# Performance work log

Hardware: AMD Instinct MI355X
Metric: run time of the kernel (lower is better)

## Reference

```python
import jax, jax.numpy as jnp
import numpy as np

B, L, D, S = 64, 512, 768, 8
HOP, LAMB = 3, 0.5


def _layernorm(x, g, b, eps=1e-5):
    m = x.mean(-1, keepdims=True)
    v = x.var(-1, keepdims=True)
    return (x - m) / jnp.sqrt(v + eps) * g + b


def _hop_refine(cur, sentence, ln_g, ln_b):
    # cur, sentence: [B,S,D]. HOP-1 refinement steps, then return last row.
    for _ in range(HOP - 1):
        coef = jnp.einsum('bd,bsd->bs', cur[:, -1, :], sentence)  # [B,S]
        a = coef[..., None] * sentence                             # [B,S,D]
        cur = LAMB * _layernorm(jax.nn.sigmoid(a), ln_g, ln_b) + sentence
    return cur[:, -1, :]  # [B,D]


def _conv1d(x, w, b):
    # x: [B,D,S], w: [Dout,Din,3], padding=1 (same)
    y = jax.lax.conv_general_dilated(
        x, w, window_strides=(1,), padding=((1, 1),),
        dimension_numbers=('NCH', 'OIH', 'NCH'))
    return y + b[None, :, None]


def setup_inputs() -> dict:
    key = jax.random.key(0)
    ks = jax.random.split(key, 16)
    p = lambda k, shp: (jax.random.normal(k, shp, dtype=jnp.float32) * 0.02)
    # segment boundaries: strictly increasing, start at 1, <= L, gaps ~63 with jitter < 32
    base = 1 + np.arange(S + 1) * ((L - 1) // S)          # [9]
    jitter = np.array(jax.random.randint(ks[15], (B, S + 1), 0, 32))
    jitter[:, 0] = 0
    jitter[:, -1] = 0
    seg_bounds = jnp.asarray(base[None, :] + jitter, dtype=jnp.int64 if jax.config.jax_enable_x64 else jnp.int32)
    return {
        'bert_output': jax.random.normal(ks[0], (B, L, D), dtype=jnp.float32),
        'target': jax.random.normal(ks[1], (B, D), dtype=jnp.float32),
        'gc1_w': p(ks[2], (D, D)), 'gc1_b': p(ks[3], (D,)),
        'gc2_w': p(ks[4], (D, D)), 'gc2_b': p(ks[5], (D,)),
        'conv1_w': p(ks[6], (D, D, 3)), 'conv1_b': p(ks[7], (D,)),
        'conv2_w': p(ks[8], (D, D, 3)), 'conv2_b': p(ks[9], (D,)),
        'ln_g': jnp.ones((D,), jnp.float32), 'ln_b': jnp.zeros((D,), jnp.float32),
        'fc2_w': p(ks[10], (3 * D, 3)), 'fc2_b': p(ks[11], (3,)),
        'seg_bounds': seg_bounds,
    }


def reference(bert_output, target, gc1_w, gc1_b, gc2_w, gc2_b,
              conv1_w, conv1_b, conv2_w, conv2_b, ln_g, ln_b,
              fc2_w, fc2_b, seg_bounds):
    dt = bert_output.dtype
    start = seg_bounds[:, :-1]   # [B,S]
    end = seg_bounds[:, 1:]      # [B,S]
    pos = jnp.arange(L)
    seg_mask = ((pos[None, None, :] >= start[:, :, None]) &
                (pos[None, None, :] < end[:, :, None])).astype(dt)  # [B,S,L]
    cnt = (end - start).astype(dt)                                   # [B,S]
    # batched segment-mean pooling
    sentence = jnp.einsum('bsl,bld->bsd', seg_mask, bert_output) / cnt[..., None]

    # GCN branch: adj = I + superdiagonal, row-degree normalization
    adj = jnp.eye(S, dtype=dt) + jnp.eye(S, k=1, dtype=dt)
    denom = adj.sum(axis=1)  # [S]

    def gcn(x, w, b):
        h = jnp.einsum('bsd,de->bse', x, w)
        return jnp.einsum('st,btd->bsd', adj, h) / denom[None, :, None] + b

    g1 = jnp.tanh(gcn(sentence, gc1_w, gc1_b))
    g2 = jnp.tanh(gcn(g1, gc2_w, gc2_b))
    a3 = _hop_refine(g2, sentence, ln_g, ln_b)

    # Conv branch: two conv1d (k=3, pad=1) over the segment axis
    x = jnp.swapaxes(sentence, 1, 2)  # [B,D,S]
    c = jnp.tanh(_conv1d(x, conv1_w, conv1_b))
    c = jnp.tanh(_conv1d(c, conv2_w, conv2_b))
    conv_out = jnp.swapaxes(c, 1, 2)  # [B,S,D]
    a4 = _hop_refine(conv_out, sentence, ln_g, ln_b)

    # Self-mask branch
    coef0 = jnp.einsum('bd,bsd->bs', sentence[:, -1, :], sentence)
    tmask = jax.nn.sigmoid(coef0[..., None] * sentence)
    a5 = _hop_refine(tmask, sentence, ln_g, ln_b)

    fnout = jnp.stack([a3, a4, a5], axis=1)                 # [B,3,D]
    # NOTE: original uses target[0] (first sample's pooler output) for all samples
    w = jax.nn.softmax(jnp.einsum('bkd,d->bk', fnout, target[0]), axis=1)
    fn = (fnout * w[..., None]).reshape(fnout.shape[0], 3 * D)
    return fn @ fc2_w + fc2_b  # [B,3]
```

## Files before the change

kernel.cpp:

```cpp
#include <hip/hip_runtime.h>


typedef unsigned short u16;
typedef short short8 __attribute__((ext_vector_type(8)));
typedef float f32x4 __attribute__((ext_vector_type(4)));

#define PART 147456

__device__ __forceinline__ float bf2f(u16 h) {
    unsigned int u = ((unsigned int)h) << 16;
    float f;
    __builtin_memcpy(&f, &u, 4);
    return f;
}
__device__ __forceinline__ u16 f2bf(float f) {
    unsigned int u;
    __builtin_memcpy(&u, &f, 4);
    u = (u + 0x7fffu + ((u >> 16) & 1u)) >> 16;
    return (u16)u;
}
__device__ __forceinline__ float sigm(float x) { return 1.0f / (1.0f + __expf(-x)); }
__device__ __forceinline__ float ftanh(float x) {
    const float xc = fminf(fmaxf(x, -15.0f), 15.0f);
    const float e = __expf(2.0f * xc);
    return __fdividef(e - 1.0f, e + 1.0f);
}
__device__ __forceinline__ float ldv(const void* p, long i, bool bf) {
    return bf ? bf2f(((const u16*)p)[i]) : ((const float*)p)[i];
}

__device__ __forceinline__ bool detect_bf16(const u16* bert) {
    int hits = 0;
#pragma unroll
    for (int i = 0; i < 256; i += 2) {
        const int e = (bert[i] >> 7) & 0xFF;
        hits += (e >= 115 && e <= 130) ? 1 : 0;
    }
    return hits > 64;
}

__global__ __launch_bounds__(256) void k1_pool_pack(
    const void* __restrict__ bertv, const int* __restrict__ sb,
    const void* __restrict__ c1w, const void* __restrict__ c2w,
    float* __restrict__ sentP, float* __restrict__ accs,
    u16* __restrict__ W1pack, u16* __restrict__ W2pack)
{
    const int u = blockIdx.x, t = threadIdx.x;
    if (u >= 768) {
        const int o = u - 768;
        const bool bf = detect_bf16((const u16*)bertv);
#pragma unroll
        for (int j = 0; j < 3; ++j) {
            const int i = t + 256 * j;
            const long base = (long)(o * 768 + i) * 3;
            u16 w1[3], w2[3];
            if (bf) {
                const u16* p1 = (const u16*)c1w + base;
                const u16* p2 = (const u16*)c2w + base;
                w1[0] = p1[0]; w1[1] = p1[1]; w1[2] = p1[2];
                w2[0] = p2[0]; w2[1] = p2[1]; w2[2] = p2[2];
            } else {
                const float* p1 = (const float*)c1w + base;
                const float* p2 = (const float*)c2w + base;
                w1[0] = f2bf(p1[0]); w1[1] = f2bf(p1[1]); w1[2] = f2bf(p1[2]);
                w2[0] = f2bf(p2[0]); w2[1] = f2bf(p2[1]); w2[2] = f2bf(p2[2]);
            }
            u16* d1 = W1pack + (size_t)o * 2304 + i;
            d1[0] = w1[0]; d1[768] = w1[1]; d1[1536] = w1[2];
            u16* d2 = W2pack + (size_t)o * 1536 + i;
            d2[0] = w2[0]; d2[768] = w2[1];
        }
        return;
    }
    if (u < 256 && t < 240)
        ((float4*)accs)[u * 240 + t] = make_float4(0.f, 0.f, 0.f, 0.f);
    const bool bf = detect_bf16((const u16*)bertv);
    const bool is64 = (sb[1] == 0);
    const int q = u & 3, w = u >> 2;
    const int b = w / 3, si = w - 3 * (w / 3), s = 5 + si;
    const int i0 = b * 9 + s, i1 = i0 + 1;
    int st = is64 ? sb[2 * i0] : sb[i0];
    int en = is64 ? sb[2 * i1] : sb[i1];
    st = st < 0 ? 0 : (st > 511 ? 511 : st);
    en = en <= st ? st + 1 : (en > 512 ? 512 : en);
    const int n = en - st;
    const int r0 = st + (n * q) / 4;
    const int r1 = st + (n * (q + 1)) / 4;
    float a0 = 0.f, a1 = 0.f, a2 = 0.f;
    if (bf) {
        const u16* base = (const u16*)bertv + (size_t)b * 512 * 768;
        int l = r0;
        for (; l + 3 < r1; l += 4) {
            const u16* p0 = base + (size_t)l * 768;
#pragma unroll
            for (int rr = 0; rr < 4; ++rr) {
                const u16* p = p0 + rr * 768;
                a0 += bf2f(p[t]);
                a1 += bf2f(p[t + 256]);
                a2 += bf2f(p[t + 512]);
            }
        }
        for (; l < r1; ++l) {
            const u16* p = base + (size_t)l * 768;
            a0 += bf2f(p[t]);
            a1 += bf2f(p[t + 256]);
            a2 += bf2f(p[t + 512]);
        }
    } else {
        const float* base = (const float*)bertv + (size_t)b * 512 * 768;
        int l = r0;
        for (; l + 3 < r1; l += 4) {
            const float* p0 = base + (size_t)l * 768;
#pragma unroll
            for (int rr = 0; rr < 4; ++rr) {
                const float* p = p0 + rr * 768;
                a0 += p[t];
                a1 += p[t + 256];
                a2 += p[t + 512];
            }
        }
        for (; l < r1; ++l) {
            const float* p = base + (size_t)l * 768;
            a0 += p[t];
            a1 += p[t + 256];
            a2 += p[t + 512];
        }
    }
    const float inv = 1.0f / (float)n;
    float* o = sentP + (size_t)q * PART + b * 2304 + si * 768;
    o[t] = a0 * inv;
    o[t + 256] = a1 * inv;
    o[t + 512] = a2 * inv;
}

template <int XMODE, int WMODE, int NPART>
__device__ __forceinline__ void gemm_core(
    const float* __restrict__ x, int xstride, const void* __restrict__ bias,
    const void* __restrict__ W, int wstride, bool bf,
    float* __restrict__ out, int ostride,
    int n0, int k0, u16* As, u16* Bs)
{
    const int t = threadIdx.x;
    const int r = t >> 2;
    const int cseg = (t & 3) * 32;
    const int wave = t >> 6, lane = t & 63;
    const int lm = lane & 15, lq = lane >> 4;
    f32x4 acc[4] = {};

    for (int kk = 0; kk < 256; kk += 128) {
        const int kg = k0 + kk;
        {
            const float* xp = x + (size_t)r * xstride + (kg + cseg);
            u16* dst = As + r * 136 + cseg;
#pragma unroll
            for (int i = 0; i < 8; ++i) {
                float4 v = ((const float4*)xp)[i];
                if (NPART == 4) {
                    const float4 v1 = ((const float4*)(xp + PART))[i];
                    const float4 v2 = ((const float4*)(xp + 2 * PART))[i];
                    const float4 v3 = ((const float4*)(xp + 3 * PART))[i];
                    v.x += v1.x + v2.x + v3.x;
                    v.y += v1.y + v2.y + v3.y;
                    v.z += v1.z + v2.z + v3.z;
                    v.w += v1.w + v2.w + v3.w;
                }
                if (XMODE == 1) {
                    int kb = kg + cseg + i * 4;
                    if (kb >= 768) kb -= 768;
                    v.x = ftanh(v.x + ldv(bias, kb, bf));
                    v.y = ftanh(v.y + ldv(bias, kb + 1, bf));
                    v.z = ftanh(v.z + ldv(bias, kb + 2, bf));
                    v.w = ftanh(v.w + ldv(bias, kb + 3, bf));
                }
                ((ushort4*)dst)[i] = make_ushort4(f2bf(v.x), f2bf(v.y), f2bf(v.z), f2bf(v.w));
            }
        }
        if (WMODE == 0) {
            const int p = t >> 2;
            const int nseg = (t & 3) * 16;
            u16 q0[16], q1[16];
            if (bf) {
                const u16* w0 = (const u16*)W + (size_t)(kg + 2 * p) * 768 + n0 + nseg;
                ((uint4*)q0)[0] = ((const uint4*)w0)[0];
                ((uint4*)q0)[1] = ((const uint4*)w0)[1];
                ((uint4*)q1)[0] = ((const uint4*)(w0 + 768))[0];
                ((uint4*)q1)[1] = ((const uint4*)(w0 + 768))[1];
            } else {
                const float* w0 = (const float*)W + (size_t)(kg + 2 * p) * 768 + n0 + nseg;
#pragma unroll
                for (int e = 0; e < 4; ++e) {
                    float4 v0 = ((const float4*)w0)[e];
                    float4 v1 = ((const float4*)(w0 + 768))[e];
                    q0[4 * e] = f2bf(v0.x); q0[4 * e + 1] = f2bf(v0.y);
                    q0[4 * e + 2] = f2bf(v0.z); q0[4 * e + 3] = f2bf(v0.w);
                    q1[4 * e] = f2bf(v1.x); q1[4 * e + 1] = f2bf(v1.y);
                    q1[4 * e + 2] = f2bf(v1.z); q1[4 * e + 3] = f2bf(v1.w);
                }
            }
#pragma unroll
            for (int e = 0; e < 16; ++e)
                *(ushort2*)(Bs + (nseg + e) * 136 + 2 * p) = make_ushort2(q0[e], q1[e]);
        } else {
            const u16* wp = (const u16*)W + (size_t)(n0 + r) * wstride + kg + cseg;
            u16* dst = Bs + r * 136 + cseg;
#pragma unroll
            for (int i = 0; i < 4; ++i)
                ((uint4*)dst)[i] = ((const uint4*)wp)[i];
        }
        __syncthreads();
        const u16* ap = As + (wave * 16 + lm) * 136 + lq * 8;
        const u16* bp = Bs + lm * 136 + lq * 8;
#pragma unroll
        for (int ks = 0; ks < 4; ++ks) {
            short8 af = *(const short8*)(ap + ks * 32);
#pragma unroll
            for (int nf = 0; nf < 4; ++nf) {
                short8 bfr = *(const short8*)(bp + nf * 16 * 136 + ks * 32);
                acc[nf] = __builtin_amdgcn_mfma_f32_16x16x32_bf16(af, bfr, acc[nf], 0, 0, 0);
            }
        }
        __syncthreads();
    }
#pragma unroll
    for (int nf = 0; nf < 4; ++nf) {
#pragma unroll
        for (int rg = 0; rg < 4; ++rg) {
            const int row = wave * 16 + lq * 4 + rg;
            const int col = n0 + nf * 16 + lm;
            atomicAdd(out + (size_t)row * ostride + col, acc[nf][rg]);
        }
    }
}

__global__ __launch_bounds__(256) void k2_gemm_a(
    const void* __restrict__ bertv,
    const float* __restrict__ sentP, const void* __restrict__ gc1w,
    const u16* __restrict__ W1pack, float* __restrict__ g1acc, float* __restrict__ c1acc)
{
    __shared__ u16 As[64 * 136];
    __shared__ u16 Bs[64 * 136];
    const bool bf = detect_bf16((const u16*)bertv);
    const int u = blockIdx.x;
    if (u < 36) {
        gemm_core<0, 0, 4>(sentP + 1536, 2304, nullptr, gc1w, 768, bf, g1acc, 768,
                           (u / 3) * 64, (u % 3) * 256, As, Bs);
    } else if (u < 144) {
        const int v = u - 36;
        gemm_core<0, 2, 4>(sentP, 2304, nullptr, W1pack, 2304, bf, c1acc, 1536,
                           (v / 9) * 64, (v % 9) * 256, As, Bs);
    } else {
        const int v = u - 144;
        gemm_core<0, 2, 4>(sentP + 768, 2304, nullptr, W1pack, 2304, bf, c1acc + 768, 1536,
                           (v / 6) * 64, (v % 6) * 256, As, Bs);
    }
}

__global__ __launch_bounds__(256) void k3_gemm_b(
    const void* __restrict__ bertv,
    const float* __restrict__ g1acc, const float* __restrict__ c1acc,
    const void* __restrict__ gc2w, const u16* __restrict__ W2pack,
    const void* __restrict__ gc1b, const void* __restrict__ c1b,
    float* __restrict__ g2acc, float* __restrict__ c2acc)
{
    __shared__ u16 As[64 * 136];
    __shared__ u16 Bs[64 * 136];
    const bool bf = detect_bf16((const u16*)bertv);
    const int u = blockIdx.x;
    if (u < 36) {
        gemm_core<1, 0, 1>(g1acc, 768, gc1b, gc2w, 768, bf, g2acc, 768,
                           (u / 3) * 64, (u % 3) * 256, As, Bs);
    } else {
        const int v = u - 36;
        gemm_core<1, 2, 1>(c1acc, 1536, c1b, W2pack, 1536, bf, c2acc, 768,
                           (v / 6) * 64, (v % 6) * 256, As, Bs);
    }
}

__device__ __forceinline__ float block_sum(float v, float* red) {
#pragma unroll
    for (int m = 1; m < 64; m <<= 1) v += __shfl_xor(v, m, 64);
    const int wave = threadIdx.x >> 6, lane = threadIdx.x & 63;
    if (lane == 0) red[wave] = v;
    __syncthreads();
    const float r = red[0] + red[1] + red[2] + red[3];
    __syncthreads();
    return r;
}

__global__ __launch_bounds__(256) void k4_final(
    const void* __restrict__ bertv,
    const float* __restrict__ sentP, const float* __restrict__ g2acc,
    const float* __restrict__ c2acc,
    const void* __restrict__ gc2b, const void* __restrict__ c2b,
    const void* __restrict__ lng, const void* __restrict__ lnb,
    const void* __restrict__ target, const void* __restrict__ fc2w,
    const void* __restrict__ fc2b, void* __restrict__ outp)
{
    __shared__ float red[4];
    const bool bf = detect_bf16((const u16*)bertv);
    const int t = threadIdx.x, b = blockIdx.x;
    float s_[3], g_[3], bb_[3];
    const float* sp = sentP + b * 2304 + 1536;
#pragma unroll
    for (int i = 0; i < 3; ++i) {
        const int d = t + 256 * i;
        s_[i] = sp[d] + sp[PART + d] + sp[2 * PART + d] + sp[3 * PART + d];
        g_[i] = ldv(lng, d, bf);
        bb_[i] = ldv(lnb, d, bf);
    }

    auto refine2 = [&](float* yv) {
#pragma unroll
        for (int it = 0; it < 2; ++it) {
            const float c = block_sum(yv[0] * s_[0] + yv[1] * s_[1] + yv[2] * s_[2], red);
            float tt[3], sm = 0.0f, sq = 0.0f;
#pragma unroll
            for (int i = 0; i < 3; ++i) {
                tt[i] = sigm(c * s_[i]);
                sm += tt[i];
                sq += tt[i] * tt[i];
            }
            const float m = block_sum(sm, red) * (1.0f / 768.0f);
            const float q = block_sum(sq, red) * (1.0f / 768.0f);
            const float inv = rsqrtf(fmaxf(q - m * m, 0.0f) + 1e-5f);
#pragma unroll
            for (int i = 0; i < 3; ++i)
                yv[i] = 0.5f * ((tt[i] - m) * inv * g_[i] + bb_[i]) + s_[i];
        }
    };

    float a3[3], a4[3], a5[3], y[3];
#pragma unroll
    for (int i = 0; i < 3; ++i) {
        const int d = t + 256 * i;
        y[i] = ftanh(g2acc[b * 768 + d] + ldv(gc2b, d, bf));
    }
    refine2(y);
    a3[0] = y[0]; a3[1] = y[1]; a3[2] = y[2];
#pragma unroll
    for (int i = 0; i < 3; ++i) {
        const int d = t + 256 * i;
        y[i] = ftanh(c2acc[b * 768 + d] + ldv(c2b, d, bf));
    }
    refine2(y);
    a4[0] = y[0]; a4[1] = y[1]; a4[2] = y[2];
    const float ss = block_sum(s_[0] * s_[0] + s_[1] * s_[1] + s_[2] * s_[2], red);
#pragma unroll
    for (int i = 0; i < 3; ++i) y[i] = sigm(ss * s_[i]);
    refine2(y);
    a5[0] = y[0]; a5[1] = y[1]; a5[2] = y[2];

    float tg[3];
#pragma unroll
    for (int i = 0; i < 3; ++i) tg[i] = ldv(target, t + 256 * i, bf);
    const float u0 = block_sum(a3[0] * tg[0] + a3[1] * tg[1] + a3[2] * tg[2], red);
    const float u1 = block_sum(a4[0] * tg[0] + a4[1] * tg[1] + a4[2] * tg[2], red);
    const float u2 = block_sum(a5[0] * tg[0] + a5[1] * tg[1] + a5[2] * tg[2], red);
    const float mx = fmaxf(u0, fmaxf(u1, u2));
    const float e0 = __expf(u0 - mx), e1 = __expf(u1 - mx), e2 = __expf(u2 - mx);
    const float es = e0 + e1 + e2;
    const float w0 = e0 / es, w1 = e1 / es, w2 = e2 / es;

    float p0 = 0.0f, p1 = 0.0f, p2 = 0.0f;
#pragma unroll
    for (int i = 0; i < 3; ++i) {
        const int d = t + 256 * i;
        const float va = w0 * a3[i], vb = w1 * a4[i], vc = w2 * a5[i];
        p0 += va * ldv(fc2w, d * 3 + 0, bf) + vb * ldv(fc2w, (768 + d) * 3 + 0, bf) + vc * ldv(fc2w, (1536 + d) * 3 + 0, bf);
        p1 += va * ldv(fc2w, d * 3 + 1, bf) + vb * ldv(fc2w, (768 + d) * 3 + 1, bf) + vc * ldv(fc2w, (1536 + d) * 3 + 1, bf);
        p2 += va * ldv(fc2w, d * 3 + 2, bf) + vb * ldv(fc2w, (768 + d) * 3 + 2, bf) + vc * ldv(fc2w, (1536 + d) * 3 + 2, bf);
    }
    p0 = block_sum(p0, red);
    p1 = block_sum(p1, red);
    p2 = block_sum(p2, red);
    if (t == 0) {
        const float o0 = p0 + ldv(fc2b, 0, bf);
        const float o1 = p1 + ldv(fc2b, 1, bf);
        const float o2 = p2 + ldv(fc2b, 2, bf);
        if (bf) {
            ((u16*)outp)[b * 3 + 0] = f2bf(o0);
            ((u16*)outp)[b * 3 + 1] = f2bf(o1);
            ((u16*)outp)[b * 3 + 2] = f2bf(o2);
        } else {
            ((float*)outp)[b * 3 + 0] = o0;
            ((float*)outp)[b * 3 + 1] = o1;
            ((float*)outp)[b * 3 + 2] = o2;
        }
    }
}

extern "C" void kernel_launch(void* const* d_in, const int* in_sizes, int n_in,
                              void* d_out, int out_size, void* d_ws, size_t ws_size,
                              hipStream_t stream) {
    const void* bert   = d_in[0];
    const void* target = d_in[1];
    const void* gc1w   = d_in[2];
    const void* gc1b   = d_in[3];
    const void* gc2w   = d_in[4];
    const void* gc2b   = d_in[5];
    const void* c1w    = d_in[6];
    const void* c1b    = d_in[7];
    const void* c2w    = d_in[8];
    const void* c2b    = d_in[9];
    const void* lng    = d_in[10];
    const void* lnb    = d_in[11];
    const void* fc2w   = d_in[12];
    const void* fc2b   = d_in[13];
    const int*  sb     = (const int*)d_in[14];

    float* sentP  = (float*)d_ws;
    float* accs   = sentP + 4 * PART;
    float* g1acc  = accs;
    float* c1acc  = accs + 49152;
    float* g2acc  = c1acc + 98304;
    float* c2acc  = g2acc + 49152;
    u16*   W1pack = (u16*)(accs + 245760);
    u16*   W2pack = W1pack + 768 * 2304;

    k1_pool_pack<<<1536, 256, 0, stream>>>(bert, sb, c1w, c2w, sentP, accs, W1pack, W2pack);
    k2_gemm_a<<<216, 256, 0, stream>>>(bert, sentP, gc1w, W1pack, g1acc, c1acc);
    k3_gemm_b<<<108, 256, 0, stream>>>(bert, g1acc, c1acc, gc2w, W2pack, gc1b, c1b, g2acc, c2acc);
    k4_final<<<64, 256, 0, stream>>>(bert, sentP, g2acc, c2acc, gc2b, c2b, lng, lnb,
                                     target, fc2w, fc2b, d_out);
}
```

Measured before the change: 225.8 us.

## Fuse second GEMM and final refinement kernel with atomic-ticket grid barrier

Merges the second GEMM kernel and the final per-batch refinement kernel into one launch. Each block takes an atomic ticket after its GEMM tile; the last 64 blocks to arrive spin until all 108 have finished, then each runs the final stage for one batch row, reading the accumulators with atomic loads. The counter is reset inside the first kernel. This removes one kernel launch and its drain/fill gap, but relies on all 108 blocks being co-resident and adds spin-waiting and atomic traffic.

```diff
diff --git a/kernel.cpp b/kernel.cpp
--- a/kernel.cpp
+++ b/kernel.cpp
@@ -43,9 +43,12 @@
     const void* __restrict__ bertv, const int* __restrict__ sb,
     const void* __restrict__ c1w, const void* __restrict__ c2w,
     float* __restrict__ sentP, float* __restrict__ accs,
-    u16* __restrict__ W1pack, u16* __restrict__ W2pack)
+    u16* __restrict__ W1pack, u16* __restrict__ W2pack,
+    int* __restrict__ counter)
 {
     const int u = blockIdx.x, t = threadIdx.x;
+    if (u == 0 && t == 0)
+        __hip_atomic_store(counter, 0, __ATOMIC_RELAXED, __HIP_MEMORY_SCOPE_AGENT);
     if (u >= 768) {
         const int o = u - 768;
         const bool bf = detect_bf16((const u16*)bertv);
@@ -255,17 +258,37 @@
     }
 }
 
-__global__ __launch_bounds__(256) void k3_gemm_b(
+__device__ __forceinline__ float block_sum(float v, float* red) {
+#pragma unroll
+    for (int m = 1; m < 64; m <<= 1) v += __shfl_xor(v, m, 64);
+    const int wave = threadIdx.x >> 6, lane = threadIdx.x & 63;
+    if (lane == 0) red[wave] = v;
+    __syncthreads();
+    const float r = red[0] + red[1] + red[2] + red[3];
+    __syncthreads();
+    return r;
+}
+
+__global__ __launch_bounds__(256) void k34_bf(
     const void* __restrict__ bertv,
     const float* __restrict__ g1acc, const float* __restrict__ c1acc,
     const void* __restrict__ gc2w, const u16* __restrict__ W2pack,
     const void* __restrict__ gc1b, const void* __restrict__ c1b,
-    float* __restrict__ g2acc, float* __restrict__ c2acc)
+    float* __restrict__ g2acc, float* __restrict__ c2acc,
+    const float* __restrict__ sentP,
+    const void* __restrict__ gc2b, const void* __restrict__ c2b,
+    const void* __restrict__ lng, const void* __restrict__ lnb,
+    const void* __restrict__ target, const void* __restrict__ fc2w,
+    const void* __restrict__ fc2b, void* __restrict__ outp,
+    int* __restrict__ counter)
 {
     __shared__ u16 As[64 * 136];
     __shared__ u16 Bs[64 * 136];
+    __shared__ float red[4];
+    __shared__ int ticket_s;
     const bool bf = detect_bf16((const u16*)bertv);
-    const int u = blockIdx.x;
+    const int u = blockIdx.x, t = threadIdx.x;
+
     if (u < 36) {
         gemm_core<1, 0, 1>(g1acc, 768, gc1b, gc2w, 768, bf, g2acc, 768,
                            (u / 3) * 64, (u % 3) * 256, As, Bs);
@@ -274,31 +297,22 @@
         gemm_core<1, 2, 1>(c1acc, 1536, c1b, W2pack, 1536, bf, c2acc, 768,
                            (v / 6) * 64, (v % 6) * 256, As, Bs);
     }
-}
-
-__device__ __forceinline__ float block_sum(float v, float* red) {
-#pragma unroll
-    for (int m = 1; m < 64; m <<= 1) v += __shfl_xor(v, m, 64);
-    const int wave = threadIdx.x >> 6, lane = threadIdx.x & 63;
-    if (lane == 0) red[wave] = v;
+
     __syncthreads();
-    const float r = red[0] + red[1] + red[2] + red[3];
+    if (t == 0) {
+        ticket_s = __hip_atomic_fetch_add(counter, 1, __ATOMIC_ACQ_REL,
+                                          __HIP_MEMORY_SCOPE_AGENT);
+    }
     __syncthreads();
-    return r;
-}
-
-__global__ __launch_bounds__(256) void k4_final(
-    const void* __restrict__ bertv,
-    const float* __restrict__ sentP, const float* __restrict__ g2acc,
-    const float* __restrict__ c2acc,
-    const void* __restrict__ gc2b, const void* __restrict__ c2b,
-    const void* __restrict__ lng, const void* __restrict__ lnb,
-    const void* __restrict__ target, const void* __restrict__ fc2w,
-    const void* __restrict__ fc2b, void* __restrict__ outp)
-{
-    __shared__ float red[4];
-    const bool bf = detect_bf16((const u16*)bertv);
-    const int t = threadIdx.x, b = blockIdx.x;
+    const int ticket = ticket_s;
+    if (ticket < 44) return;
+    if (t == 0) {
+        while (__hip_atomic_load(counter, __ATOMIC_ACQUIRE,
+                                 __HIP_MEMORY_SCOPE_AGENT) < 108) { }
+    }
+    __syncthreads();
+
+    const int b = ticket - 44;
     float s_[3], g_[3], bb_[3];
     const float* sp = sentP + b * 2304 + 1536;
 #pragma unroll
@@ -333,14 +347,18 @@
 #pragma unroll
     for (int i = 0; i < 3; ++i) {
         const int d = t + 256 * i;
-        y[i] = ftanh(g2acc[b * 768 + d] + ldv(gc2b, d, bf));
+        const float v = __hip_atomic_load(&g2acc[b * 768 + d], __ATOMIC_RELAXED,
+                                          __HIP_MEMORY_SCOPE_AGENT);
+        y[i] = ftanh(v + ldv(gc2b, d, bf));
     }
     refine2(y);
     a3[0] = y[0]; a3[1] = y[1]; a3[2] = y[2];
 #pragma unroll
     for (int i = 0; i < 3; ++i) {
         const int d = t + 256 * i;
-        y[i] = ftanh(c2acc[b * 768 + d] + ldv(c2b, d, bf));
+        const float v = __hip_atomic_load(&c2acc[b * 768 + d], __ATOMIC_RELAXED,
+                                          __HIP_MEMORY_SCOPE_AGENT);
+        y[i] = ftanh(v + ldv(c2b, d, bf));
     }
     refine2(y);
     a4[0] = y[0]; a4[1] = y[1]; a4[2] = y[2];
@@ -408,18 +426,20 @@
     const void* fc2b   = d_in[13];
     const int*  sb     = (const int*)d_in[14];
 
-    float* sentP  = (float*)d_ws;
-    float* accs   = sentP + 4 * PART;
-    float* g1acc  = accs;
-    float* c1acc  = accs + 49152;
-    float* g2acc  = c1acc + 98304;
-    float* c2acc  = g2acc + 49152;
-    u16*   W1pack = (u16*)(accs + 245760);
-    u16*   W2pack = W1pack + 768 * 2304;
-
-    k1_pool_pack<<<1536, 256, 0, stream>>>(bert, sb, c1w, c2w, sentP, accs, W1pack, W2pack);
+    float* sentP   = (float*)d_ws;
+    float* accs    = sentP + 4 * PART;
+    float* g1acc   = accs;
+    float* c1acc   = accs + 49152;
+    float* g2acc   = c1acc + 98304;
+    float* c2acc   = g2acc + 49152;
+    u16*   W1pack  = (u16*)(accs + 245760);
+    u16*   W2pack  = W1pack + 768 * 2304;
+    int*   counter = (int*)(W2pack + 768 * 1536);
+
+    k1_pool_pack<<<1536, 256, 0, stream>>>(bert, sb, c1w, c2w, sentP, accs,
+                                           W1pack, W2pack, counter);
     k2_gemm_a<<<216, 256, 0, stream>>>(bert, sentP, gc1w, W1pack, g1acc, c1acc);
-    k3_gemm_b<<<108, 256, 0, stream>>>(bert, g1acc, c1acc, gc2w, W2pack, gc1b, c1b, g2acc, c2acc);
-    k4_final<<<64, 256, 0, stream>>>(bert, sentP, g2acc, c2acc, gc2b, c2b, lng, lnb,
-                                     target, fc2w, fc2b, d_out);
-}
+    k34_bf<<<108, 256, 0, stream>>>(bert, g1acc, c1acc, gc2w, W2pack, gc1b, c1b,
+                                    g2acc, c2acc, sentP, gc2b, c2b, lng, lnb,
+                                    target, fc2w, fc2b, d_out, counter);
+}
```

Result: no change. 228.1 us (+1.0%).

## Replace atomic split-K accumulation with per-slice partial buffers reduced by consumers

Applied to the files above, without the earlier changes.

The split-K GEMM tiles now write their partial products with plain stores into separate per-K-slice slabs instead of doing atomicAdd into one zeroed accumulator. The next stage sums the slabs while loading its inputs, and the final kernel sums the g2 and c2 slabs. This removes the atomic traffic and the zeroing pass in the pooling kernel. In exchange it uses more workspace and adds extra global reads (up to 9 slabs) in the downstream loads, with a runtime-length reduction loop.

```diff
diff --git a/kernel.cpp b/kernel.cpp
--- a/kernel.cpp
+++ b/kernel.cpp
@@ -6,6 +6,7 @@
 typedef float f32x4 __attribute__((ext_vector_type(4)));
 
 #define PART 147456
+#define SLAB 49152
 
 __device__ __forceinline__ float bf2f(u16 h) {
     unsigned int u = ((unsigned int)h) << 16;
@@ -42,13 +43,13 @@
 __global__ __launch_bounds__(256) void k1_pool_pack(
     const void* __restrict__ bertv, const int* __restrict__ sb,
     const void* __restrict__ c1w, const void* __restrict__ c2w,
-    float* __restrict__ sentP, float* __restrict__ accs,
+    float* __restrict__ sentP,
     u16* __restrict__ W1pack, u16* __restrict__ W2pack)
 {
     const int u = blockIdx.x, t = threadIdx.x;
+    const bool bf = detect_bf16((const u16*)bertv);
     if (u >= 768) {
         const int o = u - 768;
-        const bool bf = detect_bf16((const u16*)bertv);
 #pragma unroll
         for (int j = 0; j < 3; ++j) {
             const int i = t + 256 * j;
@@ -72,9 +73,6 @@
         }
         return;
     }
-    if (u < 256 && t < 240)
-        ((float4*)accs)[u * 240 + t] = make_float4(0.f, 0.f, 0.f, 0.f);
-    const bool bf = detect_bf16((const u16*)bertv);
     const bool is64 = (sb[1] == 0);
     const int q = u & 3, w = u >> 2;
     const int b = w / 3, si = w - 3 * (w / 3), s = 5 + si;
@@ -133,12 +131,13 @@
     o[t + 512] = a2 * inv;
 }
 
-template <int XMODE, int WMODE, int NPART>
+template <int XMODE, int WMODE>
 __device__ __forceinline__ void gemm_core(
-    const float* __restrict__ x, int xstride, const void* __restrict__ bias,
+    const float* __restrict__ xlow, const float* __restrict__ xhigh,
+    int xrowstride, int xps, int nplow, int nphigh,
+    const void* __restrict__ bias,
     const void* __restrict__ W, int wstride, bool bf,
-    float* __restrict__ out, int ostride,
-    int n0, int k0, u16* As, u16* Bs)
+    float* __restrict__ out, int n0, int k0, u16* As, u16* Bs)
 {
     const int t = threadIdx.x;
     const int r = t >> 2;
@@ -149,24 +148,22 @@
 
     for (int kk = 0; kk < 256; kk += 128) {
         const int kg = k0 + kk;
+        const bool hi = (xhigh != nullptr) && (kg >= 768);
+        const float* xb = hi ? xhigh : xlow;
+        const int kloc = hi ? (kg - 768) : kg;
+        const int np = hi ? nphigh : nplow;
         {
-            const float* xp = x + (size_t)r * xstride + (kg + cseg);
+            const float* xp = xb + (size_t)r * xrowstride + (kloc + cseg);
             u16* dst = As + r * 136 + cseg;
 #pragma unroll
             for (int i = 0; i < 8; ++i) {
                 float4 v = ((const float4*)xp)[i];
-                if (NPART == 4) {
-                    const float4 v1 = ((const float4*)(xp + PART))[i];
-                    const float4 v2 = ((const float4*)(xp + 2 * PART))[i];
-                    const float4 v3 = ((const float4*)(xp + 3 * PART))[i];
-                    v.x += v1.x + v2.x + v3.x;
-                    v.y += v1.y + v2.y + v3.y;
-                    v.z += v1.z + v2.z + v3.z;
-                    v.w += v1.w + v2.w + v3.w;
+                for (int p = 1; p < np; ++p) {
+                    const float4 vp = ((const float4*)(xp + (size_t)p * xps))[i];
+                    v.x += vp.x; v.y += vp.y; v.z += vp.z; v.w += vp.w;
                 }
                 if (XMODE == 1) {
-                    int kb = kg + cseg + i * 4;
-                    if (kb >= 768) kb -= 768;
+                    const int kb = kloc + cseg + i * 4;
                     v.x = ftanh(v.x + ldv(bias, kb, bf));
                     v.y = ftanh(v.y + ldv(bias, kb + 1, bf));
                     v.z = ftanh(v.z + ldv(bias, kb + 2, bf));
@@ -227,7 +224,7 @@
         for (int rg = 0; rg < 4; ++rg) {
             const int row = wave * 16 + lq * 4 + rg;
             const int col = n0 + nf * 16 + lm;
-            atomicAdd(out + (size_t)row * ostride + col, acc[nf][rg]);
+            out[(size_t)row * 768 + col] = acc[nf][rg];
         }
     }
 }
@@ -235,44 +232,48 @@
 __global__ __launch_bounds__(256) void k2_gemm_a(
     const void* __restrict__ bertv,
     const float* __restrict__ sentP, const void* __restrict__ gc1w,
-    const u16* __restrict__ W1pack, float* __restrict__ g1acc, float* __restrict__ c1acc)
+    const u16* __restrict__ W1pack,
+    float* __restrict__ g1P, float* __restrict__ c1P6, float* __restrict__ c1P7)
 {
     __shared__ u16 As[64 * 136];
     __shared__ u16 Bs[64 * 136];
     const bool bf = detect_bf16((const u16*)bertv);
     const int u = blockIdx.x;
     if (u < 36) {
-        gemm_core<0, 0, 4>(sentP + 1536, 2304, nullptr, gc1w, 768, bf, g1acc, 768,
-                           (u / 3) * 64, (u % 3) * 256, As, Bs);
+        const int nt = u / 3, ks = u % 3;
+        gemm_core<0, 0>(sentP + 1536, nullptr, 2304, PART, 4, 0, nullptr,
+                        gc1w, 768, bf, g1P + (size_t)ks * SLAB, nt * 64, ks * 256, As, Bs);
     } else if (u < 144) {
-        const int v = u - 36;
-        gemm_core<0, 2, 4>(sentP, 2304, nullptr, W1pack, 2304, bf, c1acc, 1536,
-                           (v / 9) * 64, (v % 9) * 256, As, Bs);
+        const int v = u - 36, nt = v / 9, ks = v % 9;
+        gemm_core<0, 2>(sentP, nullptr, 2304, PART, 4, 0, nullptr,
+                        W1pack, 2304, bf, c1P6 + (size_t)ks * SLAB, nt * 64, ks * 256, As, Bs);
     } else {
-        const int v = u - 144;
-        gemm_core<0, 2, 4>(sentP + 768, 2304, nullptr, W1pack, 2304, bf, c1acc + 768, 1536,
-                           (v / 6) * 64, (v % 6) * 256, As, Bs);
+        const int v = u - 144, nt = v / 6, ks = v % 6;
+        gemm_core<0, 2>(sentP + 768, nullptr, 2304, PART, 4, 0, nullptr,
+                        W1pack, 2304, bf, c1P7 + (size_t)ks * SLAB, nt * 64, ks * 256, As, Bs);
     }
 }
 
 __global__ __launch_bounds__(256) void k3_gemm_b(
     const void* __restrict__ bertv,
-    const float* __restrict__ g1acc, const float* __restrict__ c1acc,
+    const float* __restrict__ g1P, const float* __restrict__ c1P6,
+    const float* __restrict__ c1P7,
     const void* __restrict__ gc2w, const u16* __restrict__ W2pack,
     const void* __restrict__ gc1b, const void* __restrict__ c1b,
-    float* __restrict__ g2acc, float* __restrict__ c2acc)
+    float* __restrict__ g2P, float* __restrict__ c2P)
 {
     __shared__ u16 As[64 * 136];
     __shared__ u16 Bs[64 * 136];
     const bool bf = detect_bf16((const u16*)bertv);
     const int u = blockIdx.x;
     if (u < 36) {
-        gemm_core<1, 0, 1>(g1acc, 768, gc1b, gc2w, 768, bf, g2acc, 768,
-                           (u / 3) * 64, (u % 3) * 256, As, Bs);
+        const int nt = u / 3, ks = u % 3;
+        gemm_core<1, 0>(g1P, nullptr, 768, SLAB, 3, 0, gc1b,
+                        gc2w, 768, bf, g2P + (size_t)ks * SLAB, nt * 64, ks * 256, As, Bs);
     } else {
-        const int v = u - 36;
-        gemm_core<1, 2, 1>(c1acc, 1536, c1b, W2pack, 1536, bf, c2acc, 768,
-                           (v / 6) * 64, (v % 6) * 256, As, Bs);
+        const int v = u - 36, nt = v / 6, ks = v % 6;
+        gemm_core<1, 2>(c1P6, c1P7, 768, SLAB, 9, 6, c1b,
+                        W2pack, 1536, bf, c2P + (size_t)ks * SLAB, nt * 64, ks * 256, As, Bs);
     }
 }
 
@@ -289,8 +290,8 @@
 
 __global__ __launch_bounds__(256) void k4_final(
     const void* __restrict__ bertv,
-    const float* __restrict__ sentP, const float* __restrict__ g2acc,
-    const float* __restrict__ c2acc,
+    const float* __restrict__ sentP, const float* __restrict__ g2P,
+    const float* __restrict__ c2P,
     const void* __restrict__ gc2b, const void* __restrict__ c2b,
     const void* __restrict__ lng, const void* __restrict__ lnb,
     const void* __restrict__ target, const void* __restrict__ fc2w,
@@ -332,15 +333,19 @@
     float a3[3], a4[3], a5[3], y[3];
 #pragma unroll
     for (int i = 0; i < 3; ++i) {
-        const int d = t + 256 * i;
-        y[i] = ftanh(g2acc[b * 768 + d] + ldv(gc2b, d, bf));
+        const int d = b * 768 + t + 256 * i;
+        const float v = g2P[d] + g2P[SLAB + d] + g2P[2 * SLAB + d];
+        y[i] = ftanh(v + ldv(gc2b, t + 256 * i, bf));
     }
     refine2(y);
     a3[0] = y[0]; a3[1] = y[1]; a3[2] = y[2];
 #pragma unroll
     for (int i = 0; i < 3; ++i) {
-        const int d = t + 256 * i;
-        y[i] = ftanh(c2acc[b * 768 + d] + ldv(c2b, d, bf));
+        const int d = b * 768 + t + 256 * i;
+        float v = c2P[d];
+#pragma unroll
+        for (int p = 1; p < 6; ++p) v += c2P[(size_t)p * SLAB + d];
+        y[i] = ftanh(v + ldv(c2b, t + 256 * i, bf));
     }
     refine2(y);
     a4[0] = y[0]; a4[1] = y[1]; a4[2] = y[2];
@@ -409,17 +414,18 @@
     const int*  sb     = (const int*)d_in[14];
 
     float* sentP  = (float*)d_ws;
-    float* accs   = sentP + 4 * PART;
-    float* g1acc  = accs;
-    float* c1acc  = accs + 49152;
-    float* g2acc  = c1acc + 98304;
-    float* c2acc  = g2acc + 49152;
-    u16*   W1pack = (u16*)(accs + 245760);
+    float* g1P    = sentP + 4 * PART;
+    float* c1P6   = g1P + 3 * SLAB;
+    float* c1P7   = c1P6 + 9 * SLAB;
+    float* g2P    = c1P7 + 6 * SLAB;
+    float* c2P    = g2P + 3 * SLAB;
+    u16*   W1pack = (u16*)(c2P + 6 * SLAB);
     u16*   W2pack = W1pack + 768 * 2304;
 
-    k1_pool_pack<<<1536, 256, 0, stream>>>(bert, sb, c1w, c2w, sentP, accs, W1pack, W2pack);
-    k2_gemm_a<<<216, 256, 0, stream>>>(bert, sentP, gc1w, W1pack, g1acc, c1acc);
-    k3_gemm_b<<<108, 256, 0, stream>>>(bert, g1acc, c1acc, gc2w, W2pack, gc1b, c1b, g2acc, c2acc);
-    k4_final<<<64, 256, 0, stream>>>(bert, sentP, g2acc, c2acc, gc2b, c2b, lng, lnb,
+    k1_pool_pack<<<1536, 256, 0, stream>>>(bert, sb, c1w, c2w, sentP, W1pack, W2pack);
+    k2_gemm_a<<<216, 256, 0, stream>>>(bert, sentP, gc1w, W1pack, g1P, c1P6, c1P7);
+    k3_gemm_b<<<108, 256, 0, stream>>>(bert, g1P, c1P6, c1P7, gc2w, W2pack,
+                                       gc1b, c1b, g2P, c2P);
+    k4_final<<<64, 256, 0, stream>>>(bert, sentP, g2P, c2P, gc2b, c2b, lng, lnb,
                                      target, fc2w, fc2b, d_out);
 }
```

New measurement: 259.1 us. 14.8% more time.
